# Performance work log

Hardware: AMD Instinct MI355X
Metric: run time of the kernel (lower is better)

## Reference

```python
import jax, jax.numpy as jnp
import numpy as np

L, H, Q, D, N, DFF = 8, 4, 64, 512, 2048, 2048


def setup_inputs() -> dict:
    key = jax.random.key(0)
    ks = jax.random.split(key, 7)
    # Scale params by ~1/sqrt(fan_in) so the 8-layer residual stack stays numerically sane.
    X = jax.random.normal(ks[0], (D, N), dtype=jnp.float32)
    K = jax.random.normal(ks[1], (L, H, Q, D), dtype=jnp.float32) * (1.0 / np.sqrt(D))
    V = jax.random.normal(ks[2], (L, H, D, D), dtype=jnp.float32) * (0.5 / np.sqrt(D))
    W1 = jax.random.normal(ks[3], (L, DFF, D), dtype=jnp.float32) * (1.0 / np.sqrt(D))
    b1 = jax.random.normal(ks[4], (L, DFF, 1), dtype=jnp.float32) * 0.02
    W2 = jax.random.normal(ks[5], (L, D, DFF), dtype=jnp.float32) * (1.0 / np.sqrt(DFF))
    b2 = jax.random.normal(ks[6], (L, D, 1), dtype=jnp.float32) * 0.02
    return {"X": X, "K": K, "V": V, "W1": W1, "b1": b1, "W2": W2, "b2": b2}


def _argmax_attn_all_heads(Kl, Vl, X):
    # Kl: [H,Q,D], Vl: [H,D,D], X: [D,N]
    KX = jnp.einsum('hqd,dn->hqn', Kl, X)                 # [H,Q,N]
    scores = jnp.einsum('hqn,hqm->hnm', KX, KX)           # [H,N,N]
    max_vals = jnp.max(scores, axis=2, keepdims=True)     # [H,N,1]
    mask = (scores >= max_vals - 0.5).astype(X.dtype)     # hard argmax-threshold mask
    row_sums = jnp.maximum(jnp.sum(mask, axis=2, keepdims=True), 1.0)
    active = (jnp.abs(max_vals) > 0.5).astype(X.dtype)
    weights = (mask / row_sums) * active                  # [H,N,N]
    Xw = jnp.einsum('dn,hnm->hdm', X, weights)            # X @ weights per head
    return jnp.einsum('hde,hem->dm', Vl, Xw)              # sum over heads of V @ (X @ weights)


def reference(X, K, V, W1, b1, W2, b2):
    for li in range(L):
        attn = X + _argmax_attn_all_heads(K[li], V[li], X)
        ff1 = jax.nn.relu(W1[li] @ attn + b1[li])
        X = attn + W2[li] @ ff1 + b2[li]
    return X
```

## Files before the change

### kernel.cpp

```cpp
#include <hip/hip_runtime.h>

#define LL   8
#define HH   4
#define QQ   64
#define DD   512
#define NN   2048
#define DFFC 2048
#define ENTRY_CAP (1 << 17)
#define CHUNK 8
#define APPLY_BLOCKS 2048
#define LCAP 2048
#define ZWORDS 149504

typedef short     bf16x8 __attribute__((ext_vector_type(8)));
typedef float     f32x4  __attribute__((ext_vector_type(4)));
typedef unsigned short u16;

__device__ inline void splitf(float v, u16& h, u16& l)
{
    unsigned u  = __float_as_uint(v);
    unsigned uh = u + (0x7FFFu + ((u >> 16) & 1u));
    h = (u16)(uh >> 16);
    float fh = __uint_as_float(((unsigned)h) << 16);
    float r  = v - fh;
    unsigned ur = __float_as_uint(r);
    unsigned ul = ur + (0x7FFFu + ((ur >> 16) & 1u));
    l = (u16)(ul >> 16);
}

__device__ inline unsigned mapf(float f)
{
    unsigned u = __float_as_uint(f);
    return (u >> 31) ? ~u : (u | 0x80000000u);
}
__device__ inline float unmapf(unsigned u)
{
    return (u >> 31) ? __uint_as_float(u ^ 0x80000000u) : __uint_as_float(~u);
}

template <int BIAS, int RELU, int WF32, int WSPLIT>
__global__ __launch_bounds__(512, 2) void mgemm8_k(
    const u16* __restrict__ Ahi, const u16* __restrict__ Alo,
    const u16* __restrict__ Bhi, const u16* __restrict__ Blo,
    float* __restrict__ C, u16* __restrict__ Chi, u16* __restrict__ Clo,
    const float* __restrict__ bias,
// ... 85 lines not shown
                acc[i][j] = __builtin_amdgcn_mfma_f32_16x16x32_bf16(
                    al[i], bh[j], acc[i][j], 0, 0, 0);
            }
        buf ^= 1;
    }
#undef STAGE8

    const int mBase = (int)mTile + wy * 32;
    const int nBase = (int)nTile + wx * 64;
#pragma unroll
    for (int i = 0; i < 2; i++) {
#pragma unroll
        for (int j = 0; j < 4; j++) {
            const int n = nBase + j * 16 + l15;
            const float bv = BIAS ? bias[n] : 0.0f;
#pragma unroll
            for (int r = 0; r < 4; r++) {
                const int m = mBase + i * 16 + quad * 4 + r;
                float v = acc[i][j][r] + bv;
                if (RELU) v = fmaxf(v, 0.0f);
                const long o = cOff + (long)m * ldc + n;
                if (WF32) C[o] = v;
                if (WSPLIT) {
                    u16 h, l;
                    splitf(v, h, l);
                    Chi[o] = h;
                    Clo[o] = l;
                }
            }
        }
    }
}

template <int MI, int BIAS, int RELU, int WF32, int WSPLIT>
__global__ __launch_bounds__(256, 2) void mgemm_k(
    const u16* __restrict__ Ahi, const u16* __restrict__ Alo,
    const u16* __restrict__ Bhi, const u16* __restrict__ Blo,
    float* __restrict__ C, u16* __restrict__ Chi, u16* __restrict__ Clo,
    const float* __restrict__ bias,
    int M, int N, int K, int lda, int ldb, int ldc,
    long sAoff, long sBoff, long sCoff,
    unsigned* __restrict__ zbase, int zn)
{
    constexpr int ACH = MI * 128;
    constexpr int TOT = 2 * ACH + 1024;
    __shared__ __align__(16) u16 smem[2 * TOT * 8];

    const int bz = blockIdx.z;
    Ahi += bz * sAoff;  Alo += bz * sAoff;
    Bhi += bz * sBoff;  Blo += bz * sBoff;
    const long cOff = (long)bz * sCoff;

    const int gx = gridDim.x, nwg = gx * gridDim.y;
    int lin = blockIdx.y * gx + blockIdx.x;
    lin = (lin & 7) * (nwg >> 3) + (lin >> 3);
    const int bxs = lin % gx, bys = lin / gx;

    const int tid  = threadIdx.x;

    if (zbase) {
        const int gtid = (blockIdx.y * gx + blockIdx.x) * 256 + tid;
        const int gstr = nwg * 256;
        for (int i = gtid; i < zn; i += gstr) zbase[i] = 0u;
    }

    const int wave = tid >> 6, lane = tid & 63;
    const int quad = lane >> 4, l15 = lane & 15;
    const int wy = wave >> 1, wx = wave & 1;
    const long mTile = (long)bys * (MI * 32);
    const long nTile = (long)bxs * 128;
    const int mBase = (int)mTile + wy * (MI * 16);
    const int nBase = (int)nTile + wx * 64;

    const int fsw = (l15 & 3) ^ ((l15 >> 2) & 3);
    const int cA  = (quad ^ fsw) * 8;

#define STAGE(bufi, koff)                                                     \
    {                                                                         \
        _Pragma("unroll")                                                     \
        for (int s = 0; s < TOT / 256; s++) {                                 \
            const int idx = s * 256 + tid;                                    \
            const u16* sp;  long rowb;  int ldx;  int rel;                    \
            if (idx < ACH)                { sp = Ahi; rel = idx;               rowb = 0; ldx = lda; } \
            else if (idx < 2 * ACH)       { sp = Alo; rel = idx - ACH;         rowb = 0; ldx = lda; } \
            else if (idx < 2 * ACH + 512) { sp = Bhi; rel = idx - 2 * ACH;     rowb = 1; ldx = ldb; } \
            else                          { sp = Blo; rel = idx - 2*ACH - 512; rowb = 1; ldx = ldb; } \
            const long rb = rowb ? nTile : mTile;                             \
            const int r = rel >> 2;                                           \
            const int c = (rel & 3) ^ ((r & 3) ^ ((r >> 2) & 3));             \
            const u16* g = sp + (rb + r) * (long)ldx + (koff) + c * 8;        \
            u16* lp = (u16*)smem + (bufi) * (TOT * 8) + idx * 8;              \
            __builtin_amdgcn_global_load_lds(                                 \
                (const __attribute__((address_space(1))) void*)g,             \
                (__attribute__((address_space(3))) void*)lp, 16, 0, 0);       \
        }                                                                     \
    }

    f32x4 acc[MI][4];
#pragma unroll
    for (int i = 0; i < MI; i++)
#pragma unroll
        for (int j = 0; j < 4; j++)
            acc[i][j] = (f32x4){0.f, 0.f, 0.f, 0.f};

    STAGE(0, 0)
    int buf = 0;
    const int NT = K >> 5;
    for (int t = 0; t < NT; t++) {
        __syncthreads();
        if (t + 1 < NT) STAGE(buf ^ 1, (t + 1) << 5)

        const u16* Lb = (const u16*)smem + buf * (TOT * 8);
        bf16x8 ah[MI], al[MI], bh[4], bl[4];
#pragma unroll
        for (int i = 0; i < MI; i++) {
            const int off = (wy * (MI * 16) + i * 16 + l15) * 32 + cA;
            ah[i] = *(const bf16x8*)(Lb + off);
            al[i] = *(const bf16x8*)(Lb + ACH * 8 + off);
        }
#pragma unroll
        for (int j = 0; j < 4; j++) {
            const int off = (wx * 64 + j * 16 + l15) * 32 + cA;
            bh[j] = *(const bf16x8*)(Lb + 2 * ACH * 8 + off);
            bl[j] = *(const bf16x8*)(Lb + 2 * ACH * 8 + 512 * 8 + off);
        }

#pragma unroll
        for (int i = 0; i < MI; i++)
#pragma unroll
            for (int j = 0; j < 4; j++) {
                acc[i][j] = __builtin_amdgcn_mfma_f32_16x16x32_bf16(
                    ah[i], bh[j], acc[i][j], 0, 0, 0);
                acc[i][j] = __builtin_amdgcn_mfma_f32_16x16x32_bf16(
                    ah[i], bl[j], acc[i][j], 0, 0, 0);
                acc[i][j] = __builtin_amdgcn_mfma_f32_16x16x32_bf16(
                    al[i], bh[j], acc[i][j], 0, 0, 0);
            }
        buf ^= 1;
    }
#undef STAGE

#pragma unroll
    for (int i = 0; i < MI; i++) {
#pragma unroll
        for (int j = 0; j < 4; j++) {
            const int n = nBase + j * 16 + l15;
            const float bv = BIAS ? bias[n] : 0.0f;
#pragma unroll
            for (int r = 0; r < 4; r++) {
                const int m = mBase + i * 16 + quad * 4 + r;
                float v = acc[i][j][r] + bv;
                if (RELU) v = fmaxf(v, 0.0f);
                const long o = cOff + (long)m * ldc + n;
                if (WF32) C[o] = v;
                if (WSPLIT) {
                    u16 h, l;
                    splitf(v, h, l);
                    Chi[o] = h;
                    Clo[o] = l;
                }
            }
        }
    }
}

__global__ __launch_bounds__(256, 2) void smax_k(
    const u16* __restrict__ Ghi, const u16* __restrict__ Glo,
    unsigned* __restrict__ rowmaxU, unsigned* __restrict__ tmaxU)
{
    __shared__ __align__(16) u16 gs[4096 * 8];
    const int h = blockIdx.z;
    const int lda = HH * QQ;
    const u16* Gh = Ghi + h * QQ;
    const u16* Gl = Glo + h * QQ;

    const int gx = gridDim.x, nwg = gx * gridDim.y;
    int lin = blockIdx.y * gx + blockIdx.x;
    lin = (lin & 7) * (nwg >> 3) + (lin >> 3);
    const int bxs = lin % gx, bys = lin / gx;

    const int tid  = threadIdx.x;
    const int wave = tid >> 6, lane = tid & 63;
    const int quad = lane >> 4, l15 = lane & 15;
    const int wy = wave >> 1, wx = wave & 1;
    const int rT = bys * 128, cT = bxs * 128;
    const int rB = rT + wy * 64;

#define SSTG(src, rowbase, dstbase)                                           \
    _Pragma("unroll")                                                         \
    for (int it = 0; it < 4; it++) {                                          \
        const int idx = it * 256 + tid;                                       \
        const int r = idx >> 3;                                               \
        const int c = (idx & 7) ^ (r & 7);                                    \
        __builtin_amdgcn_global_load_lds(                                     \
            (const __attribute__((address_space(1))) void*)(src + (long)((rowbase) + r) * lda + c * 8), \
// ... 34 lines not shown
#pragma unroll
        for (int i = 0; i < 4; i++)
#pragma unroll
            for (int j = 0; j < 4; j++) {
                acc[i][j] = __builtin_amdgcn_mfma_f32_16x16x32_bf16(ah[s][i], bh[s][j], acc[i][j], 0, 0, 0);
                acc[i][j] = __builtin_amdgcn_mfma_f32_16x16x32_bf16(ah[s][i], bl[s][j], acc[i][j], 0, 0, 0);
                acc[i][j] = __builtin_amdgcn_mfma_f32_16x16x32_bf16(al[s][i], bh[s][j], acc[i][j], 0, 0, 0);
            }

    const unsigned tBase = (unsigned)((((h << 4) + bys) << 4) + bxs) * 128u;
#pragma unroll
    for (int i = 0; i < 4; i++)
#pragma unroll
        for (int r = 0; r < 4; r++) {
            float mx = acc[i][0][r];
#pragma unroll
            for (int j = 1; j < 4; j++) mx = fmaxf(mx, acc[i][j][r]);
#pragma unroll
            for (int off = 1; off < 16; off <<= 1)
                mx = fmaxf(mx, __shfl_xor(mx, off, 64));
            if (l15 == 0) {
                const int lr = wy * 64 + i * 16 + quad * 4 + r;
                const unsigned mv = mapf(mx);
                atomicMax(&rowmaxU[h * NN + rT + lr], mv);
                atomicMax(&tmaxU[tBase + lr], mv);
            }
        }
}

__global__ __launch_bounds__(256) void sextract_k(
    const u16* __restrict__ Ghi, const u16* __restrict__ Glo,
    const unsigned* __restrict__ rowmaxU, const unsigned* __restrict__ tmaxU,
    int* __restrict__ rowcnt, unsigned* __restrict__ colcnt,
    unsigned int* __restrict__ entries, int* __restrict__ counter)
{
    const int h = blockIdx.z;
    const u16* Ah = Ghi + h * QQ;
    const u16* Al = Glo + h * QQ;
    const int lda = HH * QQ;

    const int gx = gridDim.x, nwg = gx * gridDim.y;
    int lin = blockIdx.y * gx + blockIdx.x;
    lin = (lin & 7) * (nwg >> 3) + (lin >> 3);
    const int bxs = lin % gx, bys = lin / gx;

    const int tid  = threadIdx.x;
    const int wave = tid >> 6, lane = tid & 63;
    const int quad = lane >> 4, l15 = lane & 15;
    const int wy = wave >> 1, wx = wave & 1;
    const int rB = bys * 128 + wy * 64;
    const int cT = bxs * 128;
    const int cB = cT + wx * 64;

    __shared__ float thrS[128];
    __shared__ int chist[128];
    __shared__ unsigned lbuf[LCAP];
    __shared__ int lcnt, gbase, anyf;
    if (tid == 0) { lcnt = 0; anyf = 0; }
    if (tid < 128) {
        chist[tid] = 0;
        float mx = unmapf(rowmaxU[h * NN + bys * 128 + tid]);
        float thr = (fabsf(mx) > 0.5f) ? mx - 0.5f : 3.402823466e38f;
        thrS[tid] = thr;
        float tm = unmapf(tmaxU[(unsigned)((((h << 4) + bys) << 4) + bxs) * 128u + tid]);
        if (tm >= thr) atomicAdd(&anyf, 1);
    }
    __syncthreads();
    if (anyf == 0) return;

    bf16x8 ah[2][4], al[2][4], bh[2][4], bl[2][4];
#pragma unroll
    for (int s = 0; s < 2; s++) {
        const int kk = s * 32 + quad * 8;
#pragma unroll
        for (int i = 0; i < 4; i++) {
            long ar = (long)(rB + i * 16 + l15) * lda + kk;
            ah[s][i] = *(const bf16x8*)(Ah + ar);
            al[s][i] = *(const bf16x8*)(Al + ar);
            long br = (long)(cB + i * 16 + l15) * lda + kk;
            bh[s][i] = *(const bf16x8*)(Ah + br);
            bl[s][i] = *(const bf16x8*)(Al + br);
        }
    }

    f32x4 acc[4][4];
#pragma unroll
    for (int i = 0; i < 4; i++)
#pragma unroll
        for (int j = 0; j < 4; j++)
            acc[i][j] = (f32x4){0.f, 0.f, 0.f, 0.f};

#pragma unroll
    for (int s = 0; s < 2; s++)
#pragma unroll
        for (int i = 0; i < 4; i++)
#pragma unroll
            for (int j = 0; j < 4; j++) {
                acc[i][j] = __builtin_amdgcn_mfma_f32_16x16x32_bf16(ah[s][i], bh[s][j], acc[i][j], 0, 0, 0);
                acc[i][j] = __builtin_amdgcn_mfma_f32_16x16x32_bf16(ah[s][i], bl[s][j], acc[i][j], 0, 0, 0);
                acc[i][j] = __builtin_amdgcn_mfma_f32_16x16x32_bf16(al[s][i], bh[s][j], acc[i][j], 0, 0, 0);
            }

#pragma unroll
    for (int i = 0; i < 4; i++) {
#pragma unroll
        for (int r = 0; r < 4; r++) {
            const int lr  = wy * 64 + i * 16 + quad * 4 + r;
            const int row = h * NN + rB + i * 16 + quad * 4 + r;
            const float thr = thrS[lr];

            int c = 0;
#pragma unroll
            for (int j = 0; j < 4; j++) c += (acc[i][j][r] >= thr) ? 1 : 0;
            int cs = c;
#pragma unroll
            for (int off = 1; off < 16; off <<= 1) cs += __shfl_xor(cs, off, 64);
            if (l15 == 0 && cs > 0) atomicAdd(&rowcnt[row], cs);

#pragma unroll
            for (int j = 0; j < 4; j++) {
                if (acc[i][j][r] >= thr) {
                    const unsigned m = (unsigned)(cB + j * 16 + l15);
                    unsigned ent = ((unsigned)row << 11) | m;
                    atomicAdd(&chist[m & 127], 1);
                    int s2 = atomicAdd(&lcnt, 1);
                    if (s2 < LCAP) {
                        lbuf[s2] = ent;
                    } else {
                        unsigned p = (unsigned)atomicAdd(counter, 1);
                        if (p < ENTRY_CAP) entries[p] = ent;
                    }
                }
            }
        }
    }

    __syncthreads();
    if (tid < 128) {
        int hc = chist[tid];
        if (hc > 0) atomicAdd(&colcnt[cT + tid], (unsigned)hc);
    }
    int n = lcnt;
    if (n > LCAP) n = LCAP;
    if (n > 0) {
        if (tid == 0) gbase = atomicAdd(counter, n);
        __syncthreads();
        for (int i2 = tid; i2 < n; i2 += 256) {
            unsigned p = (unsigned)(gbase + i2);
            if (p < ENTRY_CAP) entries[p] = lbuf[i2];
        }
    }
}

__global__ __launch_bounds__(256) void scan_k(
    const unsigned* __restrict__ colcnt, int* __restrict__ colOff,
    int* __restrict__ colCur)
{
    __shared__ int part[256];
    const int t = threadIdx.x;
    int e[8];
    int s = 0;
#pragma unroll
    for (int i = 0; i < 8; i++) { e[i] = s; s += (int)colcnt[t * 8 + i]; }
    part[t] = s;
    __syncthreads();
    for (int off = 1; off < 256; off <<= 1) {
        int x = (t >= off) ? part[t - off] : 0;
        __syncthreads();
        part[t] += x;
        __syncthreads();
    }
    int base = (t > 0) ? part[t - 1] : 0;
#pragma unroll
    for (int i = 0; i < 8; i++) {
        colOff[t * 8 + i] = base + e[i];
        colCur[t * 8 + i] = base + e[i];
    }
    if (t == 255) colOff[NN] = part[255];
}

__global__ __launch_bounds__(256) void scatter_k(
    const unsigned int* __restrict__ entries, const int* __restrict__ counter,
    unsigned int* __restrict__ csr, int* __restrict__ colCur)
{
    __shared__ int hist[NN];
    __shared__ int base[NN];
    int cnt = *counter;
    if (cnt > ENTRY_CAP) cnt = ENTRY_CAP;
    const int nb = gridDim.x;
    const int chunk = (cnt + nb - 1) / nb;
    const int s0 = blockIdx.x * chunk;
    int s1 = s0 + chunk;
    if (s1 > cnt) s1 = cnt;
    if (s0 >= s1) return;

    for (int i = threadIdx.x; i < NN; i += 256) hist[i] = 0;
    __syncthreads();
    for (int i = s0 + threadIdx.x; i < s1; i += 256)
        atomicAdd(&hist[entries[i] & 2047], 1);
    __syncthreads();
    for (int i = threadIdx.x; i < NN; i += 256) {
        int hcount = hist[i];
        base[i] = (hcount > 0) ? atomicAdd(&colCur[i], hcount) : 0;
        hist[i] = 0;
    }
    __syncthreads();
    for (int i = s0 + threadIdx.x; i < s1; i += 256) {
        unsigned v = entries[i];
        int m = v & 2047;
        int off = atomicAdd(&hist[m], 1);
        csr[base[m] + off] = v;
// ... 6 lines not shown
    int i = blockIdx.x * 256 + threadIdx.x;
    float4 v = ((const float4*)src)[i];
    ushort4 hv, lv;
    splitf(v.x, hv.x, lv.x);
    splitf(v.y, hv.y, lv.y);
    splitf(v.z, hv.z, lv.z);
    splitf(v.w, hv.w, lv.w);
    ((ushort4*)hi)[i] = hv;
    ((ushort4*)lo)[i] = lv;
}

__global__ __launch_bounds__(256) void splitc_k(
    const float* __restrict__ src, u16* __restrict__ hi, u16* __restrict__ lo,
    float* __restrict__ cpy)
{
    int i = blockIdx.x * 256 + threadIdx.x;
    float4 v = ((const float4*)src)[i];
    ((float4*)cpy)[i] = v;
    ushort4 hv, lv;
    splitf(v.x, hv.x, lv.x);
    splitf(v.y, hv.y, lv.y);
    splitf(v.z, hv.z, lv.z);
    splitf(v.w, hv.w, lv.w);
    ((ushort4*)hi)[i] = hv;
    ((ushort4*)lo)[i] = lv;
}

__global__ __launch_bounds__(256) void splitall_k(
    const float* __restrict__ K_, const float* __restrict__ V_,
    const float* __restrict__ W1_, const float* __restrict__ W2_,
    u16* __restrict__ KhiA, u16* __restrict__ KloA,
    u16* __restrict__ VhiA, u16* __restrict__ VloA,
    u16* __restrict__ W1hiA, u16* __restrict__ W1loA,
    u16* __restrict__ W2hiA, u16* __restrict__ W2loA)
{
    const int li  = blockIdx.x / 3200;
    const int sub = blockIdx.x % 3200;
    int i = sub * 256 + threadIdx.x;
    const float* s;
    u16 *h, *l;
    int off;
    if (i < 32768) {
        s = K_ + (long)li * 131072;
        h = KhiA + (long)li * 131072;  l = KloA + (long)li * 131072;
        off = i;
    } else if (i < 294912) {
        s = V_ + (long)li * 1048576;
        h = VhiA + (long)li * 1048576; l = VloA + (long)li * 1048576;
        off = i - 32768;
    } else if (i < 557056) {
        s = W1_ + (long)li * 1048576;
        h = W1hiA + (long)li * 1048576; l = W1loA + (long)li * 1048576;
        off = i - 294912;
    } else {
        s = W2_ + (long)li * 1048576;
        h = W2hiA + (long)li * 1048576; l = W2loA + (long)li * 1048576;
        off = i - 557056;
    }
    float4 v = ((const float4*)s)[off];
    ushort4 hv, lv;
    splitf(v.x, hv.x, lv.x);
    splitf(v.y, hv.y, lv.y);
    splitf(v.z, hv.z, lv.z);
    splitf(v.w, hv.w, lv.w);
    ((ushort4*)h)[off] = hv;
    ((ushort4*)l)[off] = lv;
}

__global__ void zero_k(int* __restrict__ counters)
{
    if (threadIdx.x < LL) counters[threadIdx.x] = 0;
}

__global__ __launch_bounds__(256) void apply_k(
    const unsigned int* __restrict__ csr, const int* __restrict__ colOff,
    const unsigned* __restrict__ rowmaxU, const int* __restrict__ rowcnt,
    const float* __restrict__ Yt, float* __restrict__ attnT)
{
    const int total = colOff[NN];
    const int tid = threadIdx.x;

    for (int base = blockIdx.x * CHUNK; base < total;
         base += gridDim.x * CHUNK) {
        int end = base + CHUNK;
        if (end > total) end = total;

        float a0 = 0.0f, a1 = 0.0f;
        int curM = -1;
        for (int e = base; e < end; e++) {
            unsigned v = csr[e];
            int m = v & 2047;
            int row = (int)(v >> 11);
            if (m != curM) {
                if (curM >= 0) {
                    atomicAdd(&attnT[(long)curM * DD + tid], a0);
                    atomicAdd(&attnT[(long)curM * DD + tid + 256], a1);
                }
                curM = m;
                a0 = a1 = 0.0f;
            }
            float mx = unmapf(rowmaxU[row]);
            float w = (fabsf(mx) > 0.5f)
                          ? 1.0f / fmaxf((float)rowcnt[row], 1.0f) : 0.0f;
            const float* y = Yt + (long)row * DD;
            a0 += w * y[tid];
            a1 += w * y[tid + 256];
        }
        if (curM >= 0) {
            atomicAdd(&attnT[(long)curM * DD + tid], a0);
            atomicAdd(&attnT[(long)curM * DD + tid + 256], a1);
        }
    }
}

__global__ __launch_bounds__(256) void ff2red_k(
    const float* __restrict__ Cpart, const float* __restrict__ b2,
    float* __restrict__ attnT, float* __restrict__ Xn,
    u16* __restrict__ Xhi, u16* __restrict__ Xlo)
{
    int i = blockIdx.x * 256 + threadIdx.x;
    float4 v0 = ((const float4*)(Cpart))[i];
    float4 v1 = ((const float4*)(Cpart + 1048576))[i];
    float4 v2 = ((const float4*)(Cpart + 2097152))[i];
    float4 v3 = ((const float4*)(Cpart + 3145728))[i];
    float4 bv = ((const float4*)b2)[i & 127];
    float4 rv = ((const float4*)attnT)[i];
    float4 o;
    o.x = v0.x + v1.x + v2.x + v3.x + bv.x + rv.x;
    o.y = v0.y + v1.y + v2.y + v3.y + bv.y + rv.y;
    o.z = v0.z + v1.z + v2.z + v3.z + bv.z + rv.z;
    o.w = v0.w + v1.w + v2.w + v3.w + bv.w + rv.w;
    ((float4*)Xn)[i] = o;
    ((float4*)attnT)[i] = o;
    ushort4 hv, lv;
    splitf(o.x, hv.x, lv.x);
    splitf(o.y, hv.y, lv.y);
    splitf(o.z, hv.z, lv.z);
    splitf(o.w, hv.w, lv.w);
    ((ushort4*)Xhi)[i] = hv;
    ((ushort4*)Xlo)[i] = lv;
}

__global__ __launch_bounds__(256) void transpose_k(
    const float* __restrict__ src, float* __restrict__ dst, int R, int C)
{
    __shared__ float t[32][33];
    int tx = threadIdx.x & 31, ty = threadIdx.x >> 5;
    int c0 = blockIdx.x * 32, r0 = blockIdx.y * 32;
#pragma unroll
    for (int k = 0; k < 4; k++)
        t[ty + 8 * k][tx] = src[(long)(r0 + ty + 8 * k) * C + c0 + tx];
    __syncthreads();
#pragma unroll
    for (int k = 0; k < 4; k++)
        dst[(long)(c0 + ty + 8 * k) * R + r0 + tx] = t[tx][ty + 8 * k];
}

extern "C" void kernel_launch(void* const* d_in, const int* in_sizes, int n_in,
                              void* d_out, int out_size, void* d_ws, size_t ws_size,
                              hipStream_t stream)
{
    const float* X0 = (const float*)d_in[0];
    const float* Kw = (const float*)d_in[1];
    const float* Vw = (const float*)d_in[2];
    const float* W1 = (const float*)d_in[3];
    const float* b1 = (const float*)d_in[4];
    const float* W2 = (const float*)d_in[5];
    const float* b2 = (const float*)d_in[6];
    float* out = (float*)d_out;

    float* R0    = (float*)d_ws;
    float* Yt    = R0;
    u16*   ff1hi = (u16*)(R0 + 4194304);
    u16*   ff1lo = (u16*)(R0 + 6291456);
    float* Cpart = R0 + 8388608;
    float* attnT = R0 + 12582912;

    float* ext = R0 + 13631488;
    u16* KXThi = (u16*)ext;
    u16* KXTlo = (u16*)(ext + 262144);
    float* XbufA = ext + 524288;
    float* XbufB = ext + 1572864;
    u16* Xhi  = (u16*)(ext + 2621440);
    u16* Xlo  = (u16*)(ext + 3145728);
    u16* athi = (u16*)(ext + 3670016);
    u16* atlo = (u16*)(ext + 4194304);
    unsigned int* entries = (unsigned int*)(ext + 8003584);
    unsigned int* csr     = (unsigned int*)(ext + 8134656);
    int* colOff   = (int*)(ext + 8265728);
    int* counters = (int*)(ext + 8267840);
    unsigned* rowmaxU = (unsigned*)(ext + 8267904);
    int* rowcnt   = (int*)(ext + 8276096);
    unsigned* colcnt = (unsigned*)(ext + 8284288);
    unsigned* tmaxU = (unsigned*)(ext + 8286336);
    int* colCur   = (int*)(ext + 8417408);
    u16* wbase = (u16*)(ext + 8419456);
    u16* KhiA  = wbase;
    u16* KloA  = wbase + 1048576;
    u16* VhiA  = wbase + 2097152;
    u16* VloA  = wbase + 10485760;
    u16* W1hiA = wbase + 18874368;
    u16* W1loA = wbase + 27262976;
    u16* W2hiA = wbase + 35651584;
    u16* W2loA = wbase + 44040192;

    zero_k<<<1, 64, 0, stream>>>(counters);

    splitall_k<<<dim3(LL * 3200), 256, 0, stream>>>(
        Kw, Vw, W1, W2, KhiA, KloA, VhiA, VloA, W1hiA, W1loA, W2hiA, W2loA);

    transpose_k<<<dim3(NN / 32, DD / 32), 256, 0, stream>>>(X0, XbufA, DD, NN);
    splitc_k<<<dim3(1024), 256, 0, stream>>>(XbufA, Xhi, Xlo, attnT);

    float* Xc = XbufA;
    for (int li = 0; li < LL; li++) {
        float* Xn = (li & 1) ? XbufA : XbufB;
        u16* Khi = KhiA + (long)li * 131072;
        u16* Klo = KloA + (long)li * 131072;
        u16* Vhi = VhiA + (long)li * 1048576;
        u16* Vlo = VloA + (long)li * 1048576;
        u16* W1hi = W1hiA + (long)li * 1048576;
        u16* W1lo = W1loA + (long)li * 1048576;
        u16* W2hi = W2hiA + (long)li * 1048576;
        u16* W2lo = W2loA + (long)li * 1048576;

        mgemm_k<1, 0, 0, 0, 1><<<dim3(2, 64, 1), 256, 0, stream>>>(
            Xhi, Xlo, Khi, Klo, nullptr, KXThi, KXTlo, nullptr,
            NN, HH * QQ, DD, DD, DD, HH * QQ, 0, 0, 0,
            rowmaxU, ZWORDS);

        smax_k<<<dim3(16, 16, HH), 256, 0, stream>>>(KXThi, KXTlo, rowmaxU, tmaxU);
        sextract_k<<<dim3(16, 16, HH), 256, 0, stream>>>(
            KXThi, KXTlo, rowmaxU, tmaxU, rowcnt, colcnt, entries, counters + li);
        scan_k<<<dim3(1), 256, 0, stream>>>(colcnt, colOff, colCur);
        scatter_k<<<dim3(64), 256, 0, stream>>>(entries, counters + li, csr, colCur);

        mgemm8_k<0, 0, 1, 0><<<dim3(4, 16, HH), 512, 0, stream>>>(
            Xhi, Xlo, Vhi, Vlo, Yt, nullptr, nullptr, nullptr,
            DD, DD, DD, DD, 0, (long)DD * DD, (long)NN * DD);

        apply_k<<<dim3(APPLY_BLOCKS), 256, 0, stream>>>(
            csr, colOff, rowmaxU, rowcnt, Yt, attnT);
        split_k<<<dim3(1024), 256, 0, stream>>>(attnT, athi, atlo);

        mgemm8_k<1, 1, 0, 1><<<dim3(16, 16, 1), 512, 0, stream>>>(
            athi, atlo, W1hi, W1lo, nullptr, ff1hi, ff1lo,
            b1 + (long)li * DFFC,
            DD, DD, DD, DFFC, 0, 0, 0);

        mgemm8_k<0, 0, 1, 0><<<dim3(4, 16, 4), 512, 0, stream>>>(
            ff1hi, ff1lo, W2hi, W2lo, Cpart, nullptr, nullptr, nullptr,
            512, DFFC, DFFC, DD, 512, 512, (long)NN * DD);
        ff2red_k<<<dim3(1024), 256, 0, stream>>>(
            Cpart, b2 + (long)li * DD, attnT, Xn, Xhi, Xlo);

        Xc = Xn;
    }

    transpose_k<<<dim3(DD / 32, NN / 32), 256, 0, stream>>>(Xc, out, NN, DD);
}
```

Measured before the change: 1.229 ms.

## Fuse KX and XV GEMMs, fold split-K reduction and scan into producers

Merges the KX projection GEMM and the per-head X·V GEMM into one launch, with an extra z-slice handling K and zeroing scratch. The FF2 split-K GEMM now does its own reduction: the last block per tile, found by an atomic ticket, sums the partials and applies bias, residual and the hi/lo split. The column scan moves into sextract via a last-block pattern, and the counter-zero kernel is folded into splitall. The aim is fewer launches and fewer separate memory passes per layer, at the cost of atomic ticketing and threadfence ordering.

```diff
diff --git a/kernel.cpp b/kernel.cpp
--- a/kernel.cpp
+++ b/kernel.cpp
@@ -10,7 +10,7 @@
 #define CHUNK 8
 #define APPLY_BLOCKS 2048
 #define LCAP 2048
-#define ZWORDS 149504
+#define ZWORDS 149600
 
 typedef short     bf16x8 __attribute__((ext_vector_type(8)));
 typedef float     f32x4  __attribute__((ext_vector_type(4)));
@@ -162,101 +162,99 @@
     }
 }
 
-template <int MI, int BIAS, int RELU, int WF32, int WSPLIT>
-__global__ __launch_bounds__(256, 2) void mgemm_k(
-    const u16* __restrict__ Ahi, const u16* __restrict__ Alo,
-    const u16* __restrict__ Bhi, const u16* __restrict__ Blo,
-    float* __restrict__ C, u16* __restrict__ Chi, u16* __restrict__ Clo,
-    const float* __restrict__ bias,
-    int M, int N, int K, int lda, int ldb, int ldc,
-    long sAoff, long sBoff, long sCoff,
-    unsigned* __restrict__ zbase, int zn)
-{
-    constexpr int ACH = MI * 128;
-    constexpr int TOT = 2 * ACH + 1024;
-    __shared__ __align__(16) u16 smem[2 * TOT * 8];
+__global__ __launch_bounds__(512, 2) void xv_k(
+    const u16* __restrict__ Xhi, const u16* __restrict__ Xlo,
+    const u16* __restrict__ Vhi, const u16* __restrict__ Vlo,
+    const u16* __restrict__ Khi, const u16* __restrict__ Klo,
+    float* __restrict__ Yt, u16* __restrict__ KXThi, u16* __restrict__ KXTlo,
+    unsigned* __restrict__ zbase)
+{
+    __shared__ __align__(16) u16 smem[2 * 2048 * 8];
 
     const int bz = blockIdx.z;
-    Ahi += bz * sAoff;  Alo += bz * sAoff;
-    Bhi += bz * sBoff;  Blo += bz * sBoff;
-    const long cOff = (long)bz * sCoff;
-
-    const int gx = gridDim.x, nwg = gx * gridDim.y;
-    int lin = blockIdx.y * gx + blockIdx.x;
-    lin = (lin & 7) * (nwg >> 3) + (lin >> 3);
-    const int bxs = lin % gx, bys = lin / gx;
-
-    const int tid  = threadIdx.x;
-
-    if (zbase) {
-        const int gtid = (blockIdx.y * gx + blockIdx.x) * 256 + tid;
-        const int gstr = nwg * 256;
-        for (int i = gtid; i < zn; i += gstr) zbase[i] = 0u;
-    }
-
-    const int wave = tid >> 6, lane = tid & 63;
+    const int tid = threadIdx.x;
+    const bool isK = (bz == 4);
+
+    int bx, by;
+    if (!isK) {
+        const int gx = 4, nwg = 64;
+        int lin = blockIdx.y * gx + blockIdx.x;
+        lin = (lin & 7) * (nwg >> 3) + (lin >> 3);
+        bx = lin % gx;  by = lin / gx;
+    } else {
+        const int gtid = (blockIdx.y * 4 + blockIdx.x) * 512 + tid;
+        for (int i = gtid; i < ZWORDS; i += 64 * 512) zbase[i] = 0u;
+        if (blockIdx.x >= 2) return;
+        bx = blockIdx.x;  by = blockIdx.y;
+    }
+
+    const u16* Bh = isK ? Khi : (Vhi + (long)bz * DD * DD);
+    const u16* Bl = isK ? Klo : (Vlo + (long)bz * DD * DD);
+    const int ldc = isK ? (HH * QQ) : DD;
+    const long cOff = isK ? 0 : (long)bz * NN * DD;
+
+    const int lane = tid & 63;
+    const int wave = tid >> 6;
     const int quad = lane >> 4, l15 = lane & 15;
     const int wy = wave >> 1, wx = wave & 1;
-    const long mTile = (long)bys * (MI * 32);
-    const long nTile = (long)bxs * 128;
-    const int mBase = (int)mTile + wy * (MI * 16);
-    const int nBase = (int)nTile + wx * 64;
+    const long mTile = (long)by * 128;
+    const long nTile = (long)bx * 128;
 
     const int fsw = (l15 & 3) ^ ((l15 >> 2) & 3);
     const int cA  = (quad ^ fsw) * 8;
 
-#define STAGE(bufi, koff)                                                     \
+    const int sr = tid >> 2;
+    const int sc = (tid & 3) ^ ((sr & 3) ^ ((sr >> 2) & 3));
+    const long aoff = (mTile + sr) * (long)DD + sc * 8;
+    const long boff = (nTile + sr) * (long)DD + sc * 8;
+
+#define STAGEX(bufi, koff)                                                    \
     {                                                                         \
-        _Pragma("unroll")                                                     \
-        for (int s = 0; s < TOT / 256; s++) {                                 \
-            const int idx = s * 256 + tid;                                    \
-            const u16* sp;  long rowb;  int ldx;  int rel;                    \
-            if (idx < ACH)                { sp = Ahi; rel = idx;               rowb = 0; ldx = lda; } \
-            else if (idx < 2 * ACH)       { sp = Alo; rel = idx - ACH;         rowb = 0; ldx = lda; } \
-            else if (idx < 2 * ACH + 512) { sp = Bhi; rel = idx - 2 * ACH;     rowb = 1; ldx = ldb; } \
-            else                          { sp = Blo; rel = idx - 2*ACH - 512; rowb = 1; ldx = ldb; } \
-            const long rb = rowb ? nTile : mTile;                             \
-            const int r = rel >> 2;                                           \
-            const int c = (rel & 3) ^ ((r & 3) ^ ((r >> 2) & 3));             \
-            const u16* g = sp + (rb + r) * (long)ldx + (koff) + c * 8;        \
-            u16* lp = (u16*)smem + (bufi) * (TOT * 8) + idx * 8;              \
-            __builtin_amdgcn_global_load_lds(                                 \
-                (const __attribute__((address_space(1))) void*)g,             \
-                (__attribute__((address_space(3))) void*)lp, 16, 0, 0);       \
-        }                                                                     \
-    }
-
-    f32x4 acc[MI][4];
-#pragma unroll
-    for (int i = 0; i < MI; i++)
+        u16* lb = (u16*)smem + (bufi) * (2048 * 8) + tid * 8;                 \
+        __builtin_amdgcn_global_load_lds(                                     \
+            (const __attribute__((address_space(1))) void*)(Xhi + aoff + (koff)), \
+            (__attribute__((address_space(3))) void*)(lb), 16, 0, 0);         \
+        __builtin_amdgcn_global_load_lds(                                     \
+            (const __attribute__((address_space(1))) void*)(Xlo + aoff + (koff)), \
+            (__attribute__((address_space(3))) void*)(lb + 512 * 8), 16, 0, 0); \
+        __builtin_amdgcn_global_load_lds(                                     \
+            (const __attribute__((address_space(1))) void*)(Bh + boff + (koff)), \
+            (__attribute__((address_space(3))) void*)(lb + 1024 * 8), 16, 0, 0); \
+        __builtin_amdgcn_global_load_lds(                                     \
+            (const __attribute__((address_space(1))) void*)(Bl + boff + (koff)), \
+            (__attribute__((address_space(3))) void*)(lb + 1536 * 8), 16, 0, 0); \
+    }
+
+    f32x4 acc[2][4];
+#pragma unroll
+    for (int i = 0; i < 2; i++)
 #pragma unroll
         for (int j = 0; j < 4; j++)
             acc[i][j] = (f32x4){0.f, 0.f, 0.f, 0.f};
 
-    STAGE(0, 0)
+    STAGEX(0, 0)
     int buf = 0;
-    const int NT = K >> 5;
-    for (int t = 0; t < NT; t++) {
+    for (int t = 0; t < 16; t++) {
         __syncthreads();
-        if (t + 1 < NT) STAGE(buf ^ 1, (t + 1) << 5)
-
-        const u16* Lb = (const u16*)smem + buf * (TOT * 8);
-        bf16x8 ah[MI], al[MI], bh[4], bl[4];
-#pragma unroll
-        for (int i = 0; i < MI; i++) {
-            const int off = (wy * (MI * 16) + i * 16 + l15) * 32 + cA;
+        if (t + 1 < 16) STAGEX(buf ^ 1, (t + 1) << 5)
+
+        const u16* Lb = (const u16*)smem + buf * (2048 * 8);
+        bf16x8 ah[2], al[2], bh[4], bl[4];
+#pragma unroll
+        for (int i = 0; i < 2; i++) {
+            const int off = (wy * 32 + i * 16 + l15) * 32 + cA;
             ah[i] = *(const bf16x8*)(Lb + off);
-            al[i] = *(const bf16x8*)(Lb + ACH * 8 + off);
+            al[i] = *(const bf16x8*)(Lb + 512 * 8 + off);
         }
 #pragma unroll
         for (int j = 0; j < 4; j++) {
             const int off = (wx * 64 + j * 16 + l15) * 32 + cA;
-            bh[j] = *(const bf16x8*)(Lb + 2 * ACH * 8 + off);
-            bl[j] = *(const bf16x8*)(Lb + 2 * ACH * 8 + 512 * 8 + off);
-        }
-
-#pragma unroll
-        for (int i = 0; i < MI; i++)
+            bh[j] = *(const bf16x8*)(Lb + 1024 * 8 + off);
+            bl[j] = *(const bf16x8*)(Lb + 1536 * 8 + off);
+        }
+
+#pragma unroll
+        for (int i = 0; i < 2; i++)
 #pragma unroll
             for (int j = 0; j < 4; j++) {
                 acc[i][j] = __builtin_amdgcn_mfma_f32_16x16x32_bf16(
@@ -268,29 +266,180 @@
             }
         buf ^= 1;
     }
-#undef STAGE
-
-#pragma unroll
-    for (int i = 0; i < MI; i++) {
+#undef STAGEX
+
+    const int mBase = (int)mTile + wy * 32;
+    const int nBase = (int)nTile + wx * 64;
+#pragma unroll
+    for (int i = 0; i < 2; i++) {
 #pragma unroll
         for (int j = 0; j < 4; j++) {
             const int n = nBase + j * 16 + l15;
-            const float bv = BIAS ? bias[n] : 0.0f;
 #pragma unroll
             for (int r = 0; r < 4; r++) {
                 const int m = mBase + i * 16 + quad * 4 + r;
-                float v = acc[i][j][r] + bv;
-                if (RELU) v = fmaxf(v, 0.0f);
+                const float v = acc[i][j][r];
                 const long o = cOff + (long)m * ldc + n;
-                if (WF32) C[o] = v;
-                if (WSPLIT) {
+                if (!isK) {
+                    Yt[o] = v;
+                } else {
                     u16 h, l;
                     splitf(v, h, l);
-                    Chi[o] = h;
-                    Clo[o] = l;
+                    KXThi[o] = h;
+                    KXTlo[o] = l;
                 }
             }
         }
+    }
+}
+
+__global__ __launch_bounds__(512, 2) void ff2_k(
+    const u16* __restrict__ Ahi, const u16* __restrict__ Alo,
+    const u16* __restrict__ Bhi, const u16* __restrict__ Blo,
+    float* __restrict__ Cpart, const float* __restrict__ b2,
+    float* __restrict__ attnT, float* __restrict__ Xn,
+    u16* __restrict__ Xhi, u16* __restrict__ Xlo,
+    int* __restrict__ tix)
+{
+    __shared__ __align__(16) u16 smem[2 * 2048 * 8];
+
+    const int bz = blockIdx.z;
+    Ahi += bz * 512;  Alo += bz * 512;
+    Bhi += bz * 512;  Blo += bz * 512;
+    float* Cz = Cpart + (long)bz * NN * DD;
+
+    const int gx = gridDim.x, nwg = gx * gridDim.y;
+    int lin = blockIdx.y * gx + blockIdx.x;
+    lin = (lin & 7) * (nwg >> 3) + (lin >> 3);
+    const int bx = lin % gx, by = lin / gx;
+
+    const int tid  = threadIdx.x;
+    const int lane = tid & 63;
+    const int wave = tid >> 6;
+    const int quad = lane >> 4, l15 = lane & 15;
+    const int wy = wave >> 1, wx = wave & 1;
+    const long mTile = (long)by * 128;
+    const long nTile = (long)bx * 128;
+
+    const int fsw = (l15 & 3) ^ ((l15 >> 2) & 3);
+    const int cA  = (quad ^ fsw) * 8;
+
+    const int sr = tid >> 2;
+    const int sc = (tid & 3) ^ ((sr & 3) ^ ((sr >> 2) & 3));
+    const long aoff = (mTile + sr) * (long)DFFC + sc * 8;
+    const long boff = (nTile + sr) * (long)DFFC + sc * 8;
+
+#define STAGEF(bufi, koff)                                                    \
+    {                                                                         \
+        u16* lb = (u16*)smem + (bufi) * (2048 * 8) + tid * 8;                 \
+        __builtin_amdgcn_global_load_lds(                                     \
+            (const __attribute__((address_space(1))) void*)(Ahi + aoff + (koff)), \
+            (__attribute__((address_space(3))) void*)(lb), 16, 0, 0);         \
+        __builtin_amdgcn_global_load_lds(                                     \
+            (const __attribute__((address_space(1))) void*)(Alo + aoff + (koff)), \
+            (__attribute__((address_space(3))) void*)(lb + 512 * 8), 16, 0, 0); \
+        __builtin_amdgcn_global_load_lds(                                     \
+            (const __attribute__((address_space(1))) void*)(Bhi + boff + (koff)), \
+            (__attribute__((address_space(3))) void*)(lb + 1024 * 8), 16, 0, 0); \
+        __builtin_amdgcn_global_load_lds(                                     \
+            (const __attribute__((address_space(1))) void*)(Blo + boff + (koff)), \
+            (__attribute__((address_space(3))) void*)(lb + 1536 * 8), 16, 0, 0); \
+    }
+
+    f32x4 acc[2][4];
+#pragma unroll
+    for (int i = 0; i < 2; i++)
+#pragma unroll
+        for (int j = 0; j < 4; j++)
+            acc[i][j] = (f32x4){0.f, 0.f, 0.f, 0.f};
+
+    STAGEF(0, 0)
+    int buf = 0;
+    for (int t = 0; t < 16; t++) {
+        __syncthreads();
+        if (t + 1 < 16) STAGEF(buf ^ 1, (t + 1) << 5)
+
+        const u16* Lb = (const u16*)smem + buf * (2048 * 8);
+        bf16x8 ah[2], al[2], bh[4], bl[4];
+#pragma unroll
+        for (int i = 0; i < 2; i++) {
+            const int off = (wy * 32 + i * 16 + l15) * 32 + cA;
+            ah[i] = *(const bf16x8*)(Lb + off);
+            al[i] = *(const bf16x8*)(Lb + 512 * 8 + off);
+        }
+#pragma unroll
+        for (int j = 0; j < 4; j++) {
+            const int off = (wx * 64 + j * 16 + l15) * 32 + cA;
+            bh[j] = *(const bf16x8*)(Lb + 1024 * 8 + off);
+            bl[j] = *(const bf16x8*)(Lb + 1536 * 8 + off);
+        }
+
+#pragma unroll
+        for (int i = 0; i < 2; i++)
+#pragma unroll
+            for (int j = 0; j < 4; j++) {
+                acc[i][j] = __builtin_amdgcn_mfma_f32_16x16x32_bf16(
+                    ah[i], bh[j], acc[i][j], 0, 0, 0);
+                acc[i][j] = __builtin_amdgcn_mfma_f32_16x16x32_bf16(
+                    ah[i], bl[j], acc[i][j], 0, 0, 0);
+                acc[i][j] = __builtin_amdgcn_mfma_f32_16x16x32_bf16(
+                    al[i], bh[j], acc[i][j], 0, 0, 0);
+            }
+        buf ^= 1;
+    }
+#undef STAGEF
+
+    const int mBase = (int)mTile + wy * 32;
+    const int nBase = (int)nTile + wx * 64;
+#pragma unroll
+    for (int i = 0; i < 2; i++)
+#pragma unroll
+        for (int j = 0; j < 4; j++) {
+            const int n = nBase + j * 16 + l15;
+#pragma unroll
+            for (int r = 0; r < 4; r++) {
+                const int m = mBase + i * 16 + quad * 4 + r;
+                Cz[(long)m * DD + n] = acc[i][j][r];
+            }
+        }
+
+    __threadfence();
+    __shared__ int lastZ;
+    const int tileId = by * 4 + bx;
+    if (tid == 0) lastZ = (atomicAdd(&tix[tileId], 1) == 3);
+    __syncthreads();
+    if (!lastZ) return;
+    __threadfence();
+
+    const float4* C0 = (const float4*)Cpart;
+    const float4* C1 = (const float4*)(Cpart + (long)NN * DD);
+    const float4* C2 = (const float4*)(Cpart + 2L * NN * DD);
+    const float4* C3 = (const float4*)(Cpart + 3L * NN * DD);
+    const float4* b2f = (const float4*)b2;
+    const int ncol4 = (int)(nTile >> 2);
+#pragma unroll
+    for (int it = 0; it < 8; it++) {
+        const int e  = it * 512 + tid;
+        const int r  = e >> 5;
+        const int c4 = e & 31;
+        const long o4 = (mTile + r) * 128 + ncol4 + c4;
+        float4 v0 = C0[o4], v1 = C1[o4], v2 = C2[o4], v3 = C3[o4];
+        float4 bv = b2f[ncol4 + c4];
+        float4 rv = ((const float4*)attnT)[o4];
+        float4 o;
+        o.x = v0.x + v1.x + v2.x + v3.x + bv.x + rv.x;
+        o.y = v0.y + v1.y + v2.y + v3.y + bv.y + rv.y;
+        o.z = v0.z + v1.z + v2.z + v3.z + bv.z + rv.z;
+        o.w = v0.w + v1.w + v2.w + v3.w + bv.w + rv.w;
+        ((float4*)Xn)[o4] = o;
+        ((float4*)attnT)[o4] = o;
+        ushort4 hv, lv;
+        splitf(o.x, hv.x, lv.x);
+        splitf(o.y, hv.y, lv.y);
+        splitf(o.z, hv.z, lv.z);
+        splitf(o.w, hv.w, lv.w);
+        ((ushort4*)Xhi)[o4] = hv;
+        ((ushort4*)Xlo)[o4] = lv;
     }
 }
 
@@ -391,7 +540,9 @@
     const u16* __restrict__ Ghi, const u16* __restrict__ Glo,
     const unsigned* __restrict__ rowmaxU, const unsigned* __restrict__ tmaxU,
     int* __restrict__ rowcnt, unsigned* __restrict__ colcnt,
-    unsigned int* __restrict__ entries, int* __restrict__ counter)
+    unsigned int* __restrict__ entries, int* __restrict__ counter,
+    int* __restrict__ colOff, int* __restrict__ colCur,
+    int* __restrict__ doneCnt)
 {
     const int h = blockIdx.z;
     const u16* Ah = Ghi + h * QQ;
@@ -414,7 +565,7 @@
     __shared__ float thrS[128];
     __shared__ int chist[128];
     __shared__ unsigned lbuf[LCAP];
-    __shared__ int lcnt, gbase, anyf;
+    __shared__ int lcnt, gbase, anyf, lastS;
     if (tid == 0) { lcnt = 0; anyf = 0; }
     if (tid < 128) {
         chist[tid] = 0;
@@ -425,117 +576,119 @@
         if (tm >= thr) atomicAdd(&anyf, 1);
     }
     __syncthreads();
-    if (anyf == 0) return;
-
-    bf16x8 ah[2][4], al[2][4], bh[2][4], bl[2][4];
-#pragma unroll
-    for (int s = 0; s < 2; s++) {
-        const int kk = s * 32 + quad * 8;
+
+    if (anyf != 0) {
+        bf16x8 ah[2][4], al[2][4], bh[2][4], bl[2][4];
+#pragma unroll
+        for (int s = 0; s < 2; s++) {
+            const int kk = s * 32 + quad * 8;
+#pragma unroll
+            for (int i = 0; i < 4; i++) {
+                long ar = (long)(rB + i * 16 + l15) * lda + kk;
+                ah[s][i] = *(const bf16x8*)(Ah + ar);
+                al[s][i] = *(const bf16x8*)(Al + ar);
+                long br = (long)(cB + i * 16 + l15) * lda + kk;
+                bh[s][i] = *(const bf16x8*)(Ah + br);
+                bl[s][i] = *(const bf16x8*)(Al + br);
+            }
+        }
+
+        f32x4 acc[4][4];
+#pragma unroll
+        for (int i = 0; i < 4; i++)
+#pragma unroll
+            for (int j = 0; j < 4; j++)
+                acc[i][j] = (f32x4){0.f, 0.f, 0.f, 0.f};
+
+#pragma unroll
+        for (int s = 0; s < 2; s++)
+#pragma unroll
+            for (int i = 0; i < 4; i++)
+#pragma unroll
+                for (int j = 0; j < 4; j++) {
+                    acc[i][j] = __builtin_amdgcn_mfma_f32_16x16x32_bf16(ah[s][i], bh[s][j], acc[i][j], 0, 0, 0);
+                    acc[i][j] = __builtin_amdgcn_mfma_f32_16x16x32_bf16(ah[s][i], bl[s][j], acc[i][j], 0, 0, 0);
+                    acc[i][j] = __builtin_amdgcn_mfma_f32_16x16x32_bf16(al[s][i], bh[s][j], acc[i][j], 0, 0, 0);
+                }
+
 #pragma unroll
         for (int i = 0; i < 4; i++) {
-            long ar = (long)(rB + i * 16 + l15) * lda + kk;
-            ah[s][i] = *(const bf16x8*)(Ah + ar);
-            al[s][i] = *(const bf16x8*)(Al + ar);
-            long br = (long)(cB + i * 16 + l15) * lda + kk;
-            bh[s][i] = *(const bf16x8*)(Ah + br);
-            bl[s][i] = *(const bf16x8*)(Al + br);
-        }
-    }
-
-    f32x4 acc[4][4];
-#pragma unroll
-    for (int i = 0; i < 4; i++)
-#pragma unroll
-        for (int j = 0; j < 4; j++)
-            acc[i][j] = (f32x4){0.f, 0.f, 0.f, 0.f};
-
-#pragma unroll
-    for (int s = 0; s < 2; s++)
-#pragma unroll
-        for (int i = 0; i < 4; i++)
-#pragma unroll
-            for (int j = 0; j < 4; j++) {
-                acc[i][j] = __builtin_amdgcn_mfma_f32_16x16x32_bf16(ah[s][i], bh[s][j], acc[i][j], 0, 0, 0);
-                acc[i][j] = __builtin_amdgcn_mfma_f32_16x16x32_bf16(ah[s][i], bl[s][j], acc[i][j], 0, 0, 0);
-                acc[i][j] = __builtin_amdgcn_mfma_f32_16x16x32_bf16(al[s][i], bh[s][j], acc[i][j], 0, 0, 0);
-            }
-
-#pragma unroll
-    for (int i = 0; i < 4; i++) {
-#pragma unroll
-        for (int r = 0; r < 4; r++) {
-            const int lr  = wy * 64 + i * 16 + quad * 4 + r;
-            const int row = h * NN + rB + i * 16 + quad * 4 + r;
-            const float thr = thrS[lr];
-
-            int c = 0;
-#pragma unroll
-            for (int j = 0; j < 4; j++) c += (acc[i][j][r] >= thr) ? 1 : 0;
-            int cs = c;
-#pragma unroll
-            for (int off = 1; off < 16; off <<= 1) cs += __shfl_xor(cs, off, 64);
-            if (l15 == 0 && cs > 0) atomicAdd(&rowcnt[row], cs);
-
-#pragma unroll
-            for (int j = 0; j < 4; j++) {
-                if (acc[i][j][r] >= thr) {
-                    const unsigned m = (unsigned)(cB + j * 16 + l15);
-                    unsigned ent = ((unsigned)row << 11) | m;
-                    atomicAdd(&chist[m & 127], 1);
-                    int s2 = atomicAdd(&lcnt, 1);
-                    if (s2 < LCAP) {
-                        lbuf[s2] = ent;
-                    } else {
-                        unsigned p = (unsigned)atomicAdd(counter, 1);
-                        if (p < ENTRY_CAP) entries[p] = ent;
+#pragma unroll
+            for (int r = 0; r < 4; r++) {
+                const int lr  = wy * 64 + i * 16 + quad * 4 + r;
+                const int row = h * NN + rB + i * 16 + quad * 4 + r;
+                const float thr = thrS[lr];
+
+                int c = 0;
+#pragma unroll
+                for (int j = 0; j < 4; j++) c += (acc[i][j][r] >= thr) ? 1 : 0;
+                int cs = c;
+#pragma unroll
+                for (int off = 1; off < 16; off <<= 1) cs += __shfl_xor(cs, off, 64);
+                if (l15 == 0 && cs > 0) atomicAdd(&rowcnt[row], cs);
+
+#pragma unroll
+                for (int j = 0; j < 4; j++) {
+                    if (acc[i][j][r] >= thr) {
+                        const unsigned m = (unsigned)(cB + j * 16 + l15);
+                        unsigned ent = ((unsigned)row << 11) | m;
+                        atomicAdd(&chist[m & 127], 1);
+                        int s2 = atomicAdd(&lcnt, 1);
+                        if (s2 < LCAP) {
+                            lbuf[s2] = ent;
+                        } else {
+                            unsigned p = (unsigned)atomicAdd(counter, 1);
+                            if (p < ENTRY_CAP) entries[p] = ent;
+                        }
                     }
                 }
             }
         }
-    }
-
+
+        __syncthreads();
+        if (tid < 128) {
+            int hc = chist[tid];
+            if (hc > 0) atomicAdd(&colcnt[cT + tid], (unsigned)hc);
+        }
+        int n = lcnt;
+        if (n > LCAP) n = LCAP;
+        if (n > 0) {
+            if (tid == 0) gbase = atomicAdd(counter, n);
+            __syncthreads();
+            for (int i2 = tid; i2 < n; i2 += 256) {
+                unsigned p = (unsigned)(gbase + i2);
+                if (p < ENTRY_CAP) entries[p] = lbuf[i2];
+            }
+        }
+    }
+
+    __threadfence();
+    if (tid == 0) lastS = (atomicAdd(doneCnt, 1) == (16 * 16 * HH - 1));
     __syncthreads();
-    if (tid < 128) {
-        int hc = chist[tid];
-        if (hc > 0) atomicAdd(&colcnt[cT + tid], (unsigned)hc);
-    }
-    int n = lcnt;
-    if (n > LCAP) n = LCAP;
-    if (n > 0) {
-        if (tid == 0) gbase = atomicAdd(counter, n);
+    if (!lastS) return;
+    __threadfence();
+    {
+        __shared__ int part[256];
+        int e[8];
+        int s = 0;
+#pragma unroll
+        for (int i = 0; i < 8; i++) { e[i] = s; s += (int)colcnt[tid * 8 + i]; }
+        part[tid] = s;
         __syncthreads();
-        for (int i2 = tid; i2 < n; i2 += 256) {
-            unsigned p = (unsigned)(gbase + i2);
-            if (p < ENTRY_CAP) entries[p] = lbuf[i2];
-        }
-    }
-}
-
-__global__ __launch_bounds__(256) void scan_k(
-    const unsigned* __restrict__ colcnt, int* __restrict__ colOff,
-    int* __restrict__ colCur)
-{
-    __shared__ int part[256];
-    const int t = threadIdx.x;
-    int e[8];
-    int s = 0;
-#pragma unroll
-    for (int i = 0; i < 8; i++) { e[i] = s; s += (int)colcnt[t * 8 + i]; }
-    part[t] = s;
-    __syncthreads();
-    for (int off = 1; off < 256; off <<= 1) {
-        int x = (t >= off) ? part[t - off] : 0;
-        __syncthreads();
-        part[t] += x;
-        __syncthreads();
-    }
-    int base = (t > 0) ? part[t - 1] : 0;
-#pragma unroll
-    for (int i = 0; i < 8; i++) {
-        colOff[t * 8 + i] = base + e[i];
-        colCur[t * 8 + i] = base + e[i];
-    }
-    if (t == 255) colOff[NN] = part[255];
+        for (int off = 1; off < 256; off <<= 1) {
+            int x = (tid >= off) ? part[tid - off] : 0;
+            __syncthreads();
+            part[tid] += x;
+            __syncthreads();
+        }
+        int base = (tid > 0) ? part[tid - 1] : 0;
+#pragma unroll
+        for (int i = 0; i < 8; i++) {
+            colOff[tid * 8 + i] = base + e[i];
+            colCur[tid * 8 + i] = base + e[i];
+        }
+        if (tid == 255) colOff[NN] = part[255];
+    }
 }
 
 __global__ __launch_bounds__(256) void scatter_k(
@@ -608,44 +761,44 @@
     u16* __restrict__ KhiA, u16* __restrict__ KloA,
     u16* __restrict__ VhiA, u16* __restrict__ VloA,
     u16* __restrict__ W1hiA, u16* __restrict__ W1loA,
-    u16* __restrict__ W2hiA, u16* __restrict__ W2loA)
-{
-    const int li  = blockIdx.x / 3200;
-    const int sub = blockIdx.x % 3200;
-    int i = sub * 256 + threadIdx.x;
-    const float* s;
-    u16 *h, *l;
-    int off;
-    if (i < 32768) {
-        s = K_ + (long)li * 131072;
-        h = KhiA + (long)li * 131072;  l = KloA + (long)li * 131072;
-        off = i;
-    } else if (i < 294912) {
-        s = V_ + (long)li * 1048576;
-        h = VhiA + (long)li * 1048576; l = VloA + (long)li * 1048576;
-        off = i - 32768;
-    } else if (i < 557056) {
-        s = W1_ + (long)li * 1048576;
-        h = W1hiA + (long)li * 1048576; l = W1loA + (long)li * 1048576;
-        off = i - 294912;
-    } else {
-        s = W2_ + (long)li * 1048576;
-        h = W2hiA + (long)li * 1048576; l = W2loA + (long)li * 1048576;
-        off = i - 557056;
-    }
-    float4 v = ((const float4*)s)[off];
-    ushort4 hv, lv;
-    splitf(v.x, hv.x, lv.x);
-    splitf(v.y, hv.y, lv.y);
-    splitf(v.z, hv.z, lv.z);
-    splitf(v.w, hv.w, lv.w);
-    ((ushort4*)h)[off] = hv;
-    ((ushort4*)l)[off] = lv;
-}
-
-__global__ void zero_k(int* __restrict__ counters)
-{
-    if (threadIdx.x < LL) counters[threadIdx.x] = 0;
+    u16* __restrict__ W2hiA, u16* __restrict__ W2loA,
+    int* __restrict__ counters)
+{
+    if (blockIdx.x == 0 && threadIdx.x < LL) counters[threadIdx.x] = 0;
+    const int li  = blockIdx.x / 1600;
+    const int sub = blockIdx.x % 1600;
+#pragma unroll
+    for (int jj = 0; jj < 2; jj++) {
+        int i = sub * 512 + jj * 256 + threadIdx.x;
+        const float* s;
+        u16 *h, *l;
+        int off;
+        if (i < 32768) {
+            s = K_ + (long)li * 131072;
+            h = KhiA + (long)li * 131072;  l = KloA + (long)li * 131072;
+            off = i;
+        } else if (i < 294912) {
+            s = V_ + (long)li * 1048576;
+            h = VhiA + (long)li * 1048576; l = VloA + (long)li * 1048576;
+            off = i - 32768;
+        } else if (i < 557056) {
+            s = W1_ + (long)li * 1048576;
+            h = W1hiA + (long)li * 1048576; l = W1loA + (long)li * 1048576;
+            off = i - 294912;
+        } else {
+            s = W2_ + (long)li * 1048576;
+            h = W2hiA + (long)li * 1048576; l = W2loA + (long)li * 1048576;
+            off = i - 557056;
+        }
+        float4 v = ((const float4*)s)[off];
+        ushort4 hv, lv;
+        splitf(v.x, hv.x, lv.x);
+        splitf(v.y, hv.y, lv.y);
+        splitf(v.z, hv.z, lv.z);
+        splitf(v.w, hv.w, lv.w);
+        ((ushort4*)h)[off] = hv;
+        ((ushort4*)l)[off] = lv;
+    }
 }
 
 __global__ __launch_bounds__(256) void apply_k(
@@ -689,34 +842,6 @@
     }
 }
 
-__global__ __launch_bounds__(256) void ff2red_k(
-    const float* __restrict__ Cpart, const float* __restrict__ b2,
-    float* __restrict__ attnT, float* __restrict__ Xn,
-    u16* __restrict__ Xhi, u16* __restrict__ Xlo)
-{
-    int i = blockIdx.x * 256 + threadIdx.x;
-    float4 v0 = ((const float4*)(Cpart))[i];
-    float4 v1 = ((const float4*)(Cpart + 1048576))[i];
-    float4 v2 = ((const float4*)(Cpart + 2097152))[i];
-    float4 v3 = ((const float4*)(Cpart + 3145728))[i];
-    float4 bv = ((const float4*)b2)[i & 127];
-    float4 rv = ((const float4*)attnT)[i];
-    float4 o;
-    o.x = v0.x + v1.x + v2.x + v3.x + bv.x + rv.x;
-    o.y = v0.y + v1.y + v2.y + v3.y + bv.y + rv.y;
-    o.z = v0.z + v1.z + v2.z + v3.z + bv.z + rv.z;
-    o.w = v0.w + v1.w + v2.w + v3.w + bv.w + rv.w;
-    ((float4*)Xn)[i] = o;
-    ((float4*)attnT)[i] = o;
-    ushort4 hv, lv;
-    splitf(o.x, hv.x, lv.x);
-    splitf(o.y, hv.y, lv.y);
-    splitf(o.z, hv.z, lv.z);
-    splitf(o.w, hv.w, lv.w);
-    ((ushort4*)Xhi)[i] = hv;
-    ((ushort4*)Xlo)[i] = lv;
-}
-
 __global__ __launch_bounds__(256) void transpose_k(
     const float* __restrict__ src, float* __restrict__ dst, int R, int C)
 {
@@ -765,12 +890,15 @@
     unsigned int* csr     = (unsigned int*)(ext + 8134656);
     int* colOff   = (int*)(ext + 8265728);
     int* counters = (int*)(ext + 8267840);
-    unsigned* rowmaxU = (unsigned*)(ext + 8267904);
-    int* rowcnt   = (int*)(ext + 8276096);
-    unsigned* colcnt = (unsigned*)(ext + 8284288);
-    unsigned* tmaxU = (unsigned*)(ext + 8286336);
-    int* colCur   = (int*)(ext + 8417408);
-    u16* wbase = (u16*)(ext + 8419456);
+    unsigned* zb      = (unsigned*)(ext + 8267904);
+    unsigned* rowmaxU = zb;
+    int*      rowcnt  = (int*)(zb + 8192);
+    unsigned* colcnt  = zb + 16384;
+    unsigned* tmaxU   = zb + 18432;
+    int*      tix     = (int*)(zb + 149504);
+    int*      done    = (int*)(zb + 149568);
+    int* colCur = (int*)(ext + 8417536);
+    u16* wbase = (u16*)(ext + 8419584);
     u16* KhiA  = wbase;
     u16* KloA  = wbase + 1048576;
     u16* VhiA  = wbase + 2097152;
@@ -780,10 +908,9 @@
     u16* W2hiA = wbase + 35651584;
     u16* W2loA = wbase + 44040192;
 
-    zero_k<<<1, 64, 0, stream>>>(counters);
-
-    splitall_k<<<dim3(LL * 3200), 256, 0, stream>>>(
-        Kw, Vw, W1, W2, KhiA, KloA, VhiA, VloA, W1hiA, W1loA, W2hiA, W2loA);
+    splitall_k<<<dim3(LL * 1600), 256, 0, stream>>>(
+        Kw, Vw, W1, W2, KhiA, KloA, VhiA, VloA, W1hiA, W1loA, W2hiA, W2loA,
+        counters);
 
     transpose_k<<<dim3(NN / 32, DD / 32), 256, 0, stream>>>(X0, XbufA, DD, NN);
     splitc_k<<<dim3(1024), 256, 0, stream>>>(XbufA, Xhi, Xlo, attnT);
@@ -800,20 +927,14 @@
         u16* W2hi = W2hiA + (long)li * 1048576;
         u16* W2lo = W2loA + (long)li * 1048576;
 
-        mgemm_k<1, 0, 0, 0, 1><<<dim3(2, 64, 1), 256, 0, stream>>>(
-            Xhi, Xlo, Khi, Klo, nullptr, KXThi, KXTlo, nullptr,
-            NN, HH * QQ, DD, DD, DD, HH * QQ, 0, 0, 0,
-            rowmaxU, ZWORDS);
+        xv_k<<<dim3(4, 16, 5), 512, 0, stream>>>(
+            Xhi, Xlo, Vhi, Vlo, Khi, Klo, Yt, KXThi, KXTlo, zb);
 
         smax_k<<<dim3(16, 16, HH), 256, 0, stream>>>(KXThi, KXTlo, rowmaxU, tmaxU);
         sextract_k<<<dim3(16, 16, HH), 256, 0, stream>>>(
-            KXThi, KXTlo, rowmaxU, tmaxU, rowcnt, colcnt, entries, counters + li);
-        scan_k<<<dim3(1), 256, 0, stream>>>(colcnt, colOff, colCur);
+            KXThi, KXTlo, rowmaxU, tmaxU, rowcnt, colcnt, entries,
+            counters + li, colOff, colCur, done);
         scatter_k<<<dim3(64), 256, 0, stream>>>(entries, counters + li, csr, colCur);
-
-        mgemm8_k<0, 0, 1, 0><<<dim3(4, 16, HH), 512, 0, stream>>>(
-            Xhi, Xlo, Vhi, Vlo, Yt, nullptr, nullptr, nullptr,
-            DD, DD, DD, DD, 0, (long)DD * DD, (long)NN * DD);
 
         apply_k<<<dim3(APPLY_BLOCKS), 256, 0, stream>>>(
             csr, colOff, rowmaxU, rowcnt, Yt, attnT);
@@ -824,11 +945,9 @@
             b1 + (long)li * DFFC,
             DD, DD, DD, DFFC, 0, 0, 0);
 
-        mgemm8_k<0, 0, 1, 0><<<dim3(4, 16, 4), 512, 0, stream>>>(
-            ff1hi, ff1lo, W2hi, W2lo, Cpart, nullptr, nullptr, nullptr,
-            512, DFFC, DFFC, DD, 512, 512, (long)NN * DD);
-        ff2red_k<<<dim3(1024), 256, 0, stream>>>(
-            Cpart, b2 + (long)li * DD, attnT, Xn, Xhi, Xlo);
+        ff2_k<<<dim3(4, 16, 4), 512, 0, stream>>>(
+            ff1hi, ff1lo, W2hi, W2lo, Cpart, b2 + (long)li * DD,
+            attnT, Xn, Xhi, Xlo, tix);
 
         Xc = Xn;
     }
```

New measurement: 2.227 ms. +81.2%, slower.
